# Optimization experiments

Measured on AMD Instinct MI355X. Metric: run time of the kernel, lower is better.

Reference implementation:

```python
import jax, jax.numpy as jnp
import numpy as np

B, F, K = 8192, 4096, 64


def setup_inputs() -> dict:
    key = jax.random.key(0)
    kx, kv = jax.random.split(key)
    x = jax.random.normal(kx, (B, F), dtype=jnp.float32)
    # original init: uniform(-0.01, 0.01)
    v = jax.random.uniform(kv, (F, K), dtype=jnp.float32, minval=-0.01, maxval=0.01)
    return {"x": x, "v": v}


def reference(x, v):
    # sum_{i<j} <v_i, v_j> x_i x_j  ==  0.5 * sum_f ((x@v)_f^2 - (x^2 @ v^2)_f)
    xv = x @ v                      # [B, K]
    x2v2 = (x * x) @ (v * v)        # [B, K]
    res = 0.5 * jnp.sum(xv * xv - x2v2, axis=-1, keepdims=True)  # [B, 1]
    return res
```

## Files before the change

### kernel.cpp

```cpp
#include <hip/hip_runtime.h>
#include <hip/hip_bf16.h>
#include <stdint.h>


#define F_DIM 4096
#define K_DIM 64
#define B_ROWS 8192

typedef __attribute__((ext_vector_type(8))) short short8;
typedef __attribute__((ext_vector_type(4))) float float4v;
typedef __attribute__((ext_vector_type(16))) float f32x16;

typedef __attribute__((address_space(3))) uint32_t lds_u32;
typedef const __attribute__((address_space(1))) uint32_t glb_u32;

__device__ __forceinline__ void load_lds16(const void* g, void* l) {
    __builtin_amdgcn_global_load_lds((glb_u32*)(uintptr_t)g,
                                     (lds_u32*)(uint32_t)(uintptr_t)l,
                                     16, 0, 0);
}

__device__ __forceinline__ short f2bs(float f) {
    __hip_bfloat16 h = __float2bfloat16(f);
    short s;
    __builtin_memcpy(&s, &h, 2);
    return s;
}

__global__ void prep_kernel(const float* __restrict__ v,
                            short* __restrict__ vtf,
                            float* __restrict__ w) {
    __shared__ short lds_t[4][64][16];

    const int wid  = threadIdx.x >> 6;
    const int lane = threadIdx.x & 63;
    const int fc   = blockIdx.x * 4 + wid;
    const int r    = lane >> 2;
    const int k0   = (lane & 3) * 16;

    const float* src = v + (size_t)(fc * 16 + r) * K_DIM + k0;
    float vals[16];
#pragma unroll
    for (int i = 0; i < 16; i += 4) {
        float4v t = *(const float4v*)(src + i);
        vals[i] = t.x; vals[i+1] = t.y; vals[i+2] = t.z; vals[i+3] = t.w;
    }

    float sq = 0.0f;
#pragma unroll
    for (int i = 0; i < 16; ++i) sq += vals[i] * vals[i];
    sq += __shfl_xor(sq, 1, 64);
    sq += __shfl_xor(sq, 2, 64);
    if ((lane & 3) == 0) w[fc * 16 + r] = sq;

#pragma unroll
    for (int kk = 0; kk < 16; ++kk) lds_t[wid][k0 + kk][r] = f2bs(vals[kk]);
    __syncthreads();

#pragma unroll
    for (int c = 0; c < 2; ++c) {
        const short8 frag = *(const short8*)&lds_t[wid][c * 32 + (lane & 31)][8 * (lane >> 5)];
        *(short8*)(vtf + ((size_t)fc * 2 + c) * 512 + lane * 8) = frag;
    }
}

__launch_bounds__(512, 2)
__global__ void fm_main_kernel(const float* __restrict__ x,
                               const short* __restrict__ vtf,
                               const float* __restrict__ w,
                               float* __restrict__ out) {
    __shared__ __align__(16) char ring[8][4][4096];
    __shared__ __align__(16) float wlds[8][512];
    __shared__ float s2red[8][32];

    const int tid  = threadIdx.x;
    const int lane = tid & 63;
    const int wid  = tid >> 6;
    const int lrow = lane & 31;
    const int hi   = lane >> 5;
    const int row0 = blockIdx.x * 32;
    const int fbase = wid * 512;
    const int fcb2  = wid * 32;

    const float* gx_base = x + (size_t)(row0 + lrow) * F_DIM + fbase + hi * 4;

#define STAGE(t) do {                                                     \
        char* eb_ = &ring[wid][(t) & 3][0];                               \
        const float* gx_ = gx_base + (t) * 16;                            \
        load_lds16(gx_,     eb_);                                         \
        load_lds16(gx_ + 8, eb_ + 1024);                                  \
        const short* gv_ = vtf + ((size_t)(fcb2 + (t))) * 1024 + lane * 8;\
        load_lds16(gv_,       eb_ + 2048);                                \
        load_lds16(gv_ + 512, eb_ + 3072);                                \
    } while (0)

    load_lds16(w + fbase + lane * 4,       &wlds[wid][0]);
    load_lds16(w + fbase + 256 + lane * 4, &wlds[wid][256]);

    STAGE(0); STAGE(1); STAGE(2);

    f32x16 acc0{};
    f32x16 acc1{};
    float s2p = 0.0f;

    const int xoff = hi * 1024 + lrow * 16;
    const int woff = hi * 32;

#pragma unroll
    for (int t = 0; t < 32; ++t) {
        if (t + 3 < 32) STAGE(t + 3);
        if (t < 29)       asm volatile("s_waitcnt vmcnt(12)" ::: "memory");
        else if (t == 29) asm volatile("s_waitcnt vmcnt(8)"  ::: "memory");
        else if (t == 30) asm volatile("s_waitcnt vmcnt(4)"  ::: "memory");
        else              asm volatile("s_waitcnt vmcnt(0)"  ::: "memory");
        __builtin_amdgcn_sched_barrier(0);

        const char* eb = &ring[wid][t & 3][0];
        const float4v xa = *(const float4v*)(eb + xoff);
        const float4v xb = *(const float4v*)(eb + xoff + 512);
        const short8  b0 = *(const short8*)(eb + 2048 + lane * 16);
        const short8  b1 = *(const short8*)(eb + 3072 + lane * 16);
        const char* wp = (const char*)&wlds[wid][0] + t * 64 + woff;
        const float4v wa = *(const float4v*)(wp);
        const float4v wb = *(const float4v*)(wp + 16);

        s2p += xa.x*xa.x*wa.x + xa.y*xa.y*wa.y + xa.z*xa.z*wa.z + xa.w*xa.w*wa.w
             + xb.x*xb.x*wb.x + xb.y*xb.y*wb.y + xb.z*xb.z*wb.z + xb.w*xb.w*wb.w;

        short8 af;
        af[0]=f2bs(xa.x); af[1]=f2bs(xa.y); af[2]=f2bs(xa.z); af[3]=f2bs(xa.w);
        af[4]=f2bs(xb.x); af[5]=f2bs(xb.y); af[6]=f2bs(xb.z); af[7]=f2bs(xb.w);

        acc0 = __builtin_amdgcn_mfma_f32_32x32x16_bf16(af, b0, acc0, 0, 0, 0);
        acc1 = __builtin_amdgcn_mfma_f32_32x32x16_bf16(af, b1, acc1, 0, 0, 0);
    }
#undef STAGE

    s2p += __shfl_xor(s2p, 32, 64);
    if (lane < 32) s2red[wid][lrow] = s2p;

    __syncthreads();

    float (*yred)[32][64] = (float (*)[32][64])&ring[0][0][0];
    const int rbase = 4 * hi;
#pragma unroll
    for (int r = 0; r < 16; ++r) {
        const int row = (r & 3) + 8 * (r >> 2) + rbase;
        yred[wid][row][lrow]      = acc0[r];
        yred[wid][row][32 + lrow] = acc1[r];
    }
    __syncthreads();

#pragma unroll
    for (int h = 0; h < 4; ++h) {
        const int row = wid * 4 + h;
        float y = 0.0f;
#pragma unroll
        for (int s = 0; s < 8; ++s) y += yred[s][row][lane];
        float yy = y * y;
#pragma unroll
        for (int m = 32; m >= 1; m >>= 1) yy += __shfl_xor(yy, m, 64);
        if (lane == 0) {
            float s2 = 0.0f;
#pragma unroll
            for (int s = 0; s < 8; ++s) s2 += s2red[s][row];
            out[row0 + row] = 0.5f * (yy - s2);
        }
    }
}

extern "C" void kernel_launch(void* const* d_in, const int* in_sizes, int n_in,
                              void* d_out, int out_size, void* d_ws, size_t ws_size,
                              hipStream_t stream) {
    const float* x = (const float*)d_in[0];
    const float* v = (const float*)d_in[1];
    float* out = (float*)d_out;

    short* vtf = (short*)d_ws;
    float* w = (float*)((char*)d_ws + (size_t)K_DIM * F_DIM * 2);

    prep_kernel<<<F_DIM / 16 / 4, 256, 0, stream>>>(v, vtf, w);
    fm_main_kernel<<<B_ROWS / 32, 512, 0, stream>>>(x, vtf, w, out);
}
```

Baseline: 199.9 us.

## Replace LDS ring pipeline with direct global loads and interleaved feature split

Drops the asynchronous global-to-LDS ring buffer with manual vmcnt waits. Each wave now reads x, w and the bf16 V fragments straight from global memory into registers, and the feature dimension is interleaved across waves (stride 128) instead of split into contiguous per-wave chunks. Freeing most of the LDS lets the launch bound go to 4 blocks per CU, trading explicit prefetching for more occupancy and hardware latency hiding. Each lane's x reads become 32-byte pieces at stride 512B, which may coalesce less well, and there is no longer any software prefetch.

```diff
diff --git a/kernel.cpp b/kernel.cpp
--- a/kernel.cpp
+++ b/kernel.cpp
@@ -10,15 +10,6 @@
 typedef __attribute__((ext_vector_type(8))) short short8;
 typedef __attribute__((ext_vector_type(4))) float float4v;
 typedef __attribute__((ext_vector_type(16))) float f32x16;
-
-typedef __attribute__((address_space(3))) uint32_t lds_u32;
-typedef const __attribute__((address_space(1))) uint32_t glb_u32;
-
-__device__ __forceinline__ void load_lds16(const void* g, void* l) {
-    __builtin_amdgcn_global_load_lds((glb_u32*)(uintptr_t)g,
-                                     (lds_u32*)(uint32_t)(uintptr_t)l,
-                                     16, 0, 0);
-}
 
 __device__ __forceinline__ short f2bs(float f) {
     __hip_bfloat16 h = __float2bfloat16(f);
@@ -64,13 +55,12 @@
     }
 }
 
-__launch_bounds__(512, 2)
+__launch_bounds__(512, 4)
 __global__ void fm_main_kernel(const float* __restrict__ x,
                                const short* __restrict__ vtf,
                                const float* __restrict__ w,
                                float* __restrict__ out) {
-    __shared__ __align__(16) char ring[8][4][4096];
-    __shared__ __align__(16) float wlds[8][512];
+    __shared__ float yred[8][32][64];
     __shared__ float s2red[8][32];
 
     const int tid  = threadIdx.x;
@@ -79,50 +69,23 @@
     const int lrow = lane & 31;
     const int hi   = lane >> 5;
     const int row0 = blockIdx.x * 32;
-    const int fbase = wid * 512;
-    const int fcb2  = wid * 32;
 
-    const float* gx_base = x + (size_t)(row0 + lrow) * F_DIM + fbase + hi * 4;
-
-#define STAGE(t) do {                                                     \
-        char* eb_ = &ring[wid][(t) & 3][0];                               \
-        const float* gx_ = gx_base + (t) * 16;                            \
-        load_lds16(gx_,     eb_);                                         \
-        load_lds16(gx_ + 8, eb_ + 1024);                                  \
-        const short* gv_ = vtf + ((size_t)(fcb2 + (t))) * 1024 + lane * 8;\
-        load_lds16(gv_,       eb_ + 2048);                                \
-        load_lds16(gv_ + 512, eb_ + 3072);                                \
-    } while (0)
-
-    load_lds16(w + fbase + lane * 4,       &wlds[wid][0]);
-    load_lds16(w + fbase + 256 + lane * 4, &wlds[wid][256]);
-
-    STAGE(0); STAGE(1); STAGE(2);
+    const float* xrow  = x + (size_t)(row0 + lrow) * F_DIM + wid * 16 + hi * 8;
+    const float* wbase = w + wid * 16 + hi * 8;
+    const short* vbase = vtf + (size_t)wid * 1024 + (size_t)lane * 8;
 
     f32x16 acc0{};
     f32x16 acc1{};
     float s2p = 0.0f;
 
-    const int xoff = hi * 1024 + lrow * 16;
-    const int woff = hi * 32;
-
-#pragma unroll
+#pragma unroll 2
     for (int t = 0; t < 32; ++t) {
-        if (t + 3 < 32) STAGE(t + 3);
-        if (t < 29)       asm volatile("s_waitcnt vmcnt(12)" ::: "memory");
-        else if (t == 29) asm volatile("s_waitcnt vmcnt(8)"  ::: "memory");
-        else if (t == 30) asm volatile("s_waitcnt vmcnt(4)"  ::: "memory");
-        else              asm volatile("s_waitcnt vmcnt(0)"  ::: "memory");
-        __builtin_amdgcn_sched_barrier(0);
-
-        const char* eb = &ring[wid][t & 3][0];
-        const float4v xa = *(const float4v*)(eb + xoff);
-        const float4v xb = *(const float4v*)(eb + xoff + 512);
-        const short8  b0 = *(const short8*)(eb + 2048 + lane * 16);
-        const short8  b1 = *(const short8*)(eb + 3072 + lane * 16);
-        const char* wp = (const char*)&wlds[wid][0] + t * 64 + woff;
-        const float4v wa = *(const float4v*)(wp);
-        const float4v wb = *(const float4v*)(wp + 16);
+        const float4v xa = *(const float4v*)(xrow + t * 128);
+        const float4v xb = *(const float4v*)(xrow + t * 128 + 4);
+        const float4v wa = *(const float4v*)(wbase + t * 128);
+        const float4v wb = *(const float4v*)(wbase + t * 128 + 4);
+        const short8  b0 = *(const short8*)(vbase + (size_t)t * 8192);
+        const short8  b1 = *(const short8*)(vbase + (size_t)t * 8192 + 512);
 
         s2p += xa.x*xa.x*wa.x + xa.y*xa.y*wa.y + xa.z*xa.z*wa.z + xa.w*xa.w*wa.w
              + xb.x*xb.x*wb.x + xb.y*xb.y*wb.y + xb.z*xb.z*wb.z + xb.w*xb.w*wb.w;
@@ -134,14 +97,10 @@
         acc0 = __builtin_amdgcn_mfma_f32_32x32x16_bf16(af, b0, acc0, 0, 0, 0);
         acc1 = __builtin_amdgcn_mfma_f32_32x32x16_bf16(af, b1, acc1, 0, 0, 0);
     }
-#undef STAGE
 
     s2p += __shfl_xor(s2p, 32, 64);
     if (lane < 32) s2red[wid][lrow] = s2p;
 
-    __syncthreads();
-
-    float (*yred)[32][64] = (float (*)[32][64])&ring[0][0][0];
     const int rbase = 4 * hi;
 #pragma unroll
     for (int r = 0; r < 16; ++r) {
```

Result: no change. 197.7 us (-1.1%).
